# Kernel tuning notes

Measured on AMD Instinct MI355X. Metric: run time of the kernel, lower is better.

The kernel has to match this reference:

```python
import jax, jax.numpy as jnp
import numpy as np

B, T, D, H = 4, 2048, 1024, 16
HD = D // H  # 64
NEG = -np.finfo(np.float32).max


def setup_inputs() -> dict:
    key = jax.random.key(0)
    ks = jax.random.split(key, 9)
    s = 1.0 / np.sqrt(D)
    return {
        "x": jax.random.normal(ks[0], (B, T, D), jnp.float32),
        "wq": jax.random.normal(ks[1], (D, D), jnp.float32) * s,
        "bq": jax.random.normal(ks[2], (D,), jnp.float32) * 0.02,
        "wk": jax.random.normal(ks[3], (D, D), jnp.float32) * s,
        "bk": jax.random.normal(ks[4], (D,), jnp.float32) * 0.02,
        "wv": jax.random.normal(ks[5], (D, D), jnp.float32) * s,
        "bv": jax.random.normal(ks[6], (D,), jnp.float32) * 0.02,
        "wo": jax.random.normal(ks[7], (D, D), jnp.float32) * s,
        "bo": jax.random.normal(ks[8], (D,), jnp.float32) * 0.02,
    }


def reference(x, wq, bq, wk, bk, wv, bv, wo, bo):
    b, t, d = x.shape
    # separate Q, K, V projections, reshape to (B, H, T, HD)
    def proj(w, bias):
        y = x @ w + bias
        return y.reshape(b, t, H, HD).transpose(0, 2, 1, 3)
    q = proj(wq, bq)
    k = proj(wk, bk)
    v = proj(wv, bv)
    scale = 1.0 / np.sqrt(HD).astype(np.float32)
    scores = jnp.einsum("bhqd,bhkd->bhqk", q, k) * scale  # (B,H,T,T)
    # causal mask: -max_float on strictly upper triangle (matches source)
    mask = jnp.triu(jnp.full((t, t), NEG, jnp.float32), k=1)
    attn = jax.nn.softmax(scores + mask, axis=-1)
    out = jnp.einsum("bhqk,bhkd->bhqd", attn, v)
    out = out.transpose(0, 2, 1, 3).reshape(b, t, d)
    return out @ wo + bo
```

## Files before the change

### kernel.cpp

```cpp
#include <hip/hip_runtime.h>

typedef __bf16 bf16x8 __attribute__((ext_vector_type(8)));
typedef float f32x4 __attribute__((ext_vector_type(4)));

#define B_ 4
#define T_ 2048
#define D_ 1024
#define H_ 16
#define HD_ 64
#define M_ 8192
#define QSCALE 0.1803368801111204f

__device__ __forceinline__ ushort f2b(float f) {
  union { float f; unsigned u; } v; v.f = f;
  unsigned u = v.u;
  return (ushort)((u + 0x7FFFu + ((u >> 16) & 1u)) >> 16);
}

__device__ __forceinline__ unsigned pkbf(float a, float b) {
  union { float f; unsigned u; } va, vb; va.f = a; vb.f = b;
  return __builtin_amdgcn_perm(vb.u + 0x8000u, va.u + 0x8000u, 0x07060302u);
}

__device__ __forceinline__ void gll16(const void* g, void* l) {
  __builtin_amdgcn_global_load_lds(
      (const __attribute__((address_space(1))) unsigned*)g,
      (__attribute__((address_space(3))) unsigned*)l, 16, 0, 0);
}

__global__ __launch_bounds__(256) void cast_x_kernel(const float* __restrict__ x,
                                                     ushort* __restrict__ xb) {
  int idx = blockIdx.x * 256 + threadIdx.x;
  float4 v = ((const float4*)x)[idx];
  ushort4 o;
  o.x = f2b(v.x); o.y = f2b(v.y); o.z = f2b(v.z); o.w = f2b(v.w);
  ((ushort4*)xb)[idx] = o;
}

__global__ __launch_bounds__(256) void transpose_w_kernel(
    const float* __restrict__ wq, const float* __restrict__ wk,
    const float* __restrict__ wv, const float* __restrict__ wo,
    ushort* __restrict__ wt_qkv, ushort* __restrict__ wt_o) {
  __shared__ float tile[32][33];
  int z = blockIdx.z;
  const float* src = (z == 0) ? wq : (z == 1) ? wk : (z == 2) ? wv : wo;
  ushort* dst = (z < 3) ? (wt_qkv + (size_t)z * D_ * D_) : wt_o;
  int n0 = blockIdx.x * 32, k0 = blockIdx.y * 32;
  int tx = threadIdx.x & 31, ty = threadIdx.x >> 5;
  for (int i = 0; i < 4; i++) {
    int r = ty + i * 8;
    tile[r][tx] = src[(size_t)(k0 + r) * D_ + n0 + tx];
  }
  __syncthreads();
  for (int i = 0; i < 4; i++) {
    int r = ty + i * 8;
    dst[(size_t)(n0 + r) * D_ + k0 + tx] = f2b(tile[tx][r]);
  }
}

__global__ __launch_bounds__(512) void gemm_kernel(
    const ushort* __restrict__ A, const ushort* __restrict__ Bt, int mode,
    const float* __restrict__ bias_q, const float* __restrict__ bias_k,
    const float* __restrict__ bias_v,
    ushort* __restrict__ qb, ushort* __restrict__ kb, ushort* __restrict__ vtb,
    float* __restrict__ outf) {
  extern __shared__ char lds_raw[];
  ushort (*As)[256][64] = (ushort (*)[256][64])lds_raw;
  ushort (*Bs)[128][64] = (ushort (*)[128][64])(lds_raw + 98304);
  int tid = threadIdx.x;
  int wave = tid >> 6, lane = tid & 63, lrow = lane >> 4, lcol = lane & 15;
  int wr = wave >> 1, wc = wave & 1;

  int gx = gridDim.x;
  int nwg = gx * gridDim.y;
  int orig = blockIdx.x + gx * blockIdx.y;
  int work = (orig & 7) * (nwg >> 3) + (orig >> 3);
  int m0 = (work / gx) * 256, n0 = (work % gx) * 128;

  int r_s = tid >> 3, c_s = tid & 7;
  int scv = c_s ^ (r_s & 7);
  const ushort* aB = A + (size_t)(m0 + r_s) * D_ + scv * 8;
  const ushort* bB = Bt + (size_t)(n0 + r_s) * D_ + scv * 8;

  auto stageA = [&](int buf, int t, int u) {
    const ushort* s = aB + (size_t)u * 128 * D_ + t * 64;
    char* d = (char*)&As[buf][0][0] + u * 16384 + tid * 16;
    gll16(s, d);
    gll16(s + (size_t)64 * D_, d + 8192);
  };
  auto stageB = [&](int buf, int t) {
    const ushort* s = bB + t * 64;
    char* d = (char*)&Bs[buf][0][0] + tid * 16;
    gll16(s, d);
    gll16(s + (size_t)64 * D_, d + 8192);
  };

  f32x4 zero = {0.f, 0.f, 0.f, 0.f};
  f32x4 acc[4][4];
  for (int i = 0; i < 4; i++)
    for (int j = 0; j < 4; j++) acc[i][j] = zero;

  int swz = lcol & 7;

  stageA(0, 0, 0); stageA(0, 0, 1); stageB(0, 0);
  stageA(1, 1, 0); stageA(1, 1, 1); stageB(1, 1);
  asm volatile("s_waitcnt vmcnt(6)" ::: "memory");
  __builtin_amdgcn_sched_barrier(0);
  __builtin_amdgcn_s_barrier();

#pragma unroll
  for (int t = 0; t < 16; ++t) {
    int buf = t % 3;
    int nb = (t + 2) % 3;
#pragma unroll
    for (int ks = 0; ks < 2; ++ks) {
      bf16x8 af[4], bf[4];
      int ch = ((ks * 4 + lrow) ^ swz) * 8;
#pragma unroll
      for (int mt = 0; mt < 4; mt++)
        af[mt] = *(const bf16x8*)&As[buf][wr * 64 + mt * 16 + lcol][ch];
#pragma unroll
      for (int nt = 0; nt < 4; nt++)
        bf[nt] = *(const bf16x8*)&Bs[buf][wc * 64 + nt * 16 + lcol][ch];
      if (t + 2 < 16) {
        if (ks == 0) { stageA(nb, t + 2, 0); stageA(nb, t + 2, 1); }
        else         { stageB(nb, t + 2); }
      }
      __builtin_amdgcn_sched_barrier(0);
      __builtin_amdgcn_s_barrier();
      __builtin_amdgcn_sched_barrier(0);
      __builtin_amdgcn_s_setprio(1);
#pragma unroll
      for (int mt = 0; mt < 4; mt++)
#pragma unroll
        for (int nt = 0; nt < 4; nt++)
          acc[mt][nt] = __builtin_amdgcn_mfma_f32_16x16x32_bf16(
              af[mt], bf[nt], acc[mt][nt], 0, 0, 0);
      __builtin_amdgcn_s_setprio(0);
      if (ks == 1) {
        if (t <= 13) {
          asm volatile("s_waitcnt vmcnt(6)" ::: "memory");
        } else if (t == 14) {
          asm volatile("s_waitcnt vmcnt(0)" ::: "memory");
        }
      }
      __builtin_amdgcn_sched_barrier(0);
      __builtin_amdgcn_s_barrier();
    }
  }

  if (mode == 0) {
    int proj = n0 >> 10;
    const float* bias = (proj == 0) ? bias_q : (proj == 1) ? bias_k : bias_v;
    for (int mt = 0; mt < 4; mt++) {
      int gm0 = m0 + wr * 64 + mt * 16 + lrow * 4;
      int b = gm0 >> 11, tp = gm0 & 2047;
      for (int nt = 0; nt < 4; nt++) {
        int gn = n0 + wc * 64 + nt * 16 + lcol;
        int inner = gn & 1023;
        int h = inner >> 6, hd = inner & 63;
        float bv = bias[inner];
        if (proj == 0) {
          size_t base = ((size_t)(b * H_ + h) * T_ + tp) * HD_ + hd;
          for (int r = 0; r < 4; r++)
            qb[base + (size_t)r * HD_] = f2b((acc[mt][nt][r] + bv) * QSCALE);
        } else if (proj == 1) {
          size_t base = ((size_t)(b * H_ + h) * T_ + tp) * HD_ + hd;
          for (int r = 0; r < 4; r++)
            kb[base + (size_t)r * HD_] = f2b(acc[mt][nt][r] + bv);
        } else {
          ushort4 pk;
          pk.x = f2b(acc[mt][nt][0] + bv);
          pk.y = f2b(acc[mt][nt][1] + bv);
          pk.z = f2b(acc[mt][nt][2] + bv);
          pk.w = f2b(acc[mt][nt][3] + bv);
          *(ushort4*)&vtb[((size_t)(b * H_ + h) * HD_ + hd) * T_ + tp] = pk;
        }
      }
    }
  } else {
    for (int mt = 0; mt < 4; mt++) {
      int gm0 = m0 + wr * 64 + mt * 16 + lrow * 4;
      for (int nt = 0; nt < 4; nt++) {
        int gn = n0 + wc * 64 + nt * 16 + lcol;
        float bv = bias_q[gn];
        for (int r = 0; r < 4; r++)
          outf[(size_t)(gm0 + r) * D_ + gn] = acc[mt][nt][r] + bv;
      }
    }
  }
}

#define QCOMP(qblk_, q0w_, qfv, accOv, accSv)                                   \
  do {                                                                          \
    f32x4 st[2][4];                                                             \
    for (int qh = 0; qh < 2; qh++)                                              \
      for (int mt = 0; mt < 4; mt++) st[qh][mt] = zero;                         \
    __builtin_amdgcn_s_setprio(1);                                              \
    _Pragma("unroll")                                                           \
    for (int ks = 0; ks < 2; ks++)                                              \
      _Pragma("unroll")                                                         \
      for (int mt = 0; mt < 4; mt++) {                                          \
        bf16x8 kf = *(const bf16x8*)&Ks2[cur][mt * 16 + lcol]                   \
                                        [((ks * 4 + lrow) ^ rsw) * 8];          \
        st[0][mt] = __builtin_amdgcn_mfma_f32_16x16x32_bf16(kf, qfv[0][ks],     \
                                                            st[0][mt], 0, 0, 0);\
        st[1][mt] = __builtin_amdgcn_mfma_f32_16x16x32_bf16(kf, qfv[1][ks],     \
                                                            st[1][mt], 0, 0, 0);\
      }                                                                         \
    __builtin_amdgcn_s_setprio(0);                                              \
    if (j >= 2 * (qblk_)) {                                                     \
      _Pragma("unroll")                                                         \
      for (int qh = 0; qh < 2; qh++) {                                          \
        int q_g = (q0w_) + qh * 16 + lcol;                                      \
        _Pragma("unroll")                                                       \
        for (int mt = 0; mt < 4; mt++)                                          \
          for (int r = 0; r < 4; r++) {                                         \
            int kv_g = j * 64 + mt * 16 + lrow * 4 + r;                         \
            if (kv_g > q_g) st[qh][mt][r] = -1e30f;                             \
          }                                                                     \
      }                                                                         \
    }                                                                           \
    _Pragma("unroll")                                                           \
    for (int qh = 0; qh < 2; qh++)                                              \
      for (int mt = 0; mt < 4; mt++)                                            \
        for (int r = 0; r < 4; r++)                                             \
          st[qh][mt][r] = __builtin_amdgcn_exp2f(st[qh][mt][r]);                \
    _Pragma("unroll")                                                           \
    for (int qh = 0; qh < 2; qh++)                                              \
      for (int mt = 0; mt < 4; mt++) {                                          \
        uint2 pk;                                                               \
        pk.x = pkbf(st[qh][mt][0], st[qh][mt][1]);                              \
        pk.y = pkbf(st[qh][mt][2], st[qh][mt][3]);                              \
        int sl = ((2 * mt + (lrow >> 1)) ^ rsw) * 8 + (lrow & 1) * 4;           \
        *(uint2*)&Ps[wave][qh * 16 + lcol][sl] = pk;                            \
      }                                                                         \
    __builtin_amdgcn_s_setprio(1);                                              \
    _Pragma("unroll")                                                           \
    for (int ks = 0; ks < 2; ks++) {                                            \
      int ch = ((ks * 4 + lrow) ^ rsw) * 8;                                     \
      bf16x8 pf0 = *(const bf16x8*)&Ps[wave][lcol][ch];                         \
      bf16x8 pf1 = *(const bf16x8*)&Ps[wave][16 + lcol][ch];                    \
      accSv[0] = __builtin_amdgcn_mfma_f32_16x16x32_bf16(af1, pf0, accSv[0],    \
                                                         0, 0, 0);              \
      accSv[1] = __builtin_amdgcn_mfma_f32_16x16x32_bf16(af1, pf1, accSv[1],    \
                                                         0, 0, 0);              \
      _Pragma("unroll")                                                         \
      for (int mt = 0; mt < 4; mt++) {                                          \
        bf16x8 vf = *(const bf16x8*)&Vs2[cur][mt * 16 + lcol][ch];              \
        accOv[0][mt] = __builtin_amdgcn_mfma_f32_16x16x32_bf16(vf, pf0,         \
                                                    accOv[0][mt], 0, 0, 0);     \
        accOv[1][mt] = __builtin_amdgcn_mfma_f32_16x16x32_bf16(vf, pf1,         \
                                                    accOv[1][mt], 0, 0, 0);     \
      }                                                                         \
    }                                                                           \
    __builtin_amdgcn_s_setprio(0);                                              \
  } while (0)

__global__ __launch_bounds__(256) void flash_kernel(
    const ushort* __restrict__ qb, const ushort* __restrict__ kb,
    const ushort* __restrict__ vtb, ushort* __restrict__ ob) {
  __shared__ ushort Ks2[2][64][64];
  __shared__ ushort Vs2[2][64][64];
  __shared__ ushort Ps[4][32][64];
  int tid = threadIdx.x;
  int wave = tid >> 6, lane = tid & 63, lrow = lane >> 4, lcol = lane & 15;

  int bid = blockIdx.x + (blockIdx.y << 3);
  int xcd = bid & 7;
  int slot = bid >> 3;
  int phase = slot >> 5;
  int j5 = slot & 31;
  int pm = j5 & 7;
  int bh = xcd * 8 + (j5 >> 3) + phase * 4;
  int p = phase ? 7 - pm : pm;
  int qbA = 15 - p, qbB = p;
  int b = bh >> 4, h = bh & 15;
  const ushort* qp = qb + (size_t)bh * T_ * HD_;
  const ushort* kh = kb + (size_t)bh * T_ * HD_;
  const ushort* vh = vtb + (size_t)bh * HD_ * T_;

  int njA = 2 * qbA + 2, njB = 2 * qbB + 2;

  int r0 = tid >> 3, dc = tid & 7;
  int wsl = (dc ^ (r0 & 7)) * 8;
  int rsw = lcol & 7;

  uint4 kr0, kr1, vr0, vr1;
  auto gload = [&](int jt) {
    kr0 = *(const uint4*)&kh[(size_t)(jt * 64 + r0) * HD_ + dc * 8];
    kr1 = *(const uint4*)&kh[(size_t)(jt * 64 + r0 + 32) * HD_ + dc * 8];
    vr0 = *(const uint4*)&vh[(size_t)r0 * T_ + jt * 64 + dc * 8];
    vr1 = *(const uint4*)&vh[(size_t)(r0 + 32) * T_ + jt * 64 + dc * 8];
  };
  auto swrite = [&](int buf) {
    *(uint4*)&Ks2[buf][r0][wsl] = kr0;
    *(uint4*)&Ks2[buf][r0 + 32][wsl] = kr1;
    *(uint4*)&Vs2[buf][r0][wsl] = vr0;
    *(uint4*)&Vs2[buf][r0 + 32][wsl] = vr1;
  };

  bf16x8 af1;
  {
    __bf16 ov = (__bf16)((lcol == 0) ? 1.0f : 0.0f);
    for (int i2 = 0; i2 < 8; i2++) af1[i2] = ov;
  }

  f32x4 zero = {0.f, 0.f, 0.f, 0.f};

  gload(0);
  swrite(0);
  gload(1);
  __syncthreads();

  int q0wA = qbA * 128 + wave * 32, q0wB = qbB * 128 + wave * 32;
  bf16x8 qfA[2][2], qfB[2][2];
#pragma unroll
  for (int qh = 0; qh < 2; qh++)
#pragma unroll
    for (int ks = 0; ks < 2; ks++) {
      qfA[qh][ks] = *(const bf16x8*)&qp[(size_t)(q0wA + qh * 16 + lcol) * HD_ +
                                        ks * 32 + lrow * 8];
      qfB[qh][ks] = *(const bf16x8*)&qp[(size_t)(q0wB + qh * 16 + lcol) * HD_ +
                                        ks * 32 + lrow * 8];
    }

  f32x4 accOA[2][4], accOB[2][4];
  f32x4 accSA[2], accSB[2];
#pragma unroll
  for (int qh = 0; qh < 2; qh++) {
    accSA[qh] = zero; accSB[qh] = zero;
    for (int mt = 0; mt < 4; mt++) { accOA[qh][mt] = zero; accOB[qh][mt] = zero; }
  }

  for (int j = 0; j < njA; j++) {
    int cur = j & 1;
    if (j * 64 <= q0wA + 31) QCOMP(qbA, q0wA, qfA, accOA, accSA);
    if (j * 64 <= q0wB + 31) QCOMP(qbB, q0wB, qfB, accOB, accSB);
    if (j + 1 < njA) swrite(cur ^ 1);
    if (j + 2 < njA) gload(j + 2);
    __syncthreads();
  }
  (void)njB;

#pragma unroll
  for (int qh = 0; qh < 2; qh++) {
    float lsum = __shfl(accSA[qh][0], lcol);
    float linv = 1.f / lsum;
    int t = q0wA + qh * 16 + lcol;
    size_t base2 = ((size_t)b * T_ + t) * D_ + h * HD_;
#pragma unroll
    for (int mt = 0; mt < 4; mt++) {
      uint2 pk;
      pk.x = pkbf(accOA[qh][mt][0] * linv, accOA[qh][mt][1] * linv);
      pk.y = pkbf(accOA[qh][mt][2] * linv, accOA[qh][mt][3] * linv);
      *(uint2*)&ob[base2 + mt * 16 + lrow * 4] = pk;
    }
  }
#pragma unroll
  for (int qh = 0; qh < 2; qh++) {
    float lsum = __shfl(accSB[qh][0], lcol);
    float linv = 1.f / lsum;
    int t = q0wB + qh * 16 + lcol;
    size_t base2 = ((size_t)b * T_ + t) * D_ + h * HD_;
#pragma unroll
    for (int mt = 0; mt < 4; mt++) {
      uint2 pk;
      pk.x = pkbf(accOB[qh][mt][0] * linv, accOB[qh][mt][1] * linv);
      pk.y = pkbf(accOB[qh][mt][2] * linv, accOB[qh][mt][3] * linv);
      *(uint2*)&ob[base2 + mt * 16 + lrow * 4] = pk;
    }
  }
}

extern "C" void kernel_launch(void* const* d_in, const int* in_sizes, int n_in,
                              void* d_out, int out_size, void* d_ws, size_t ws_size,
                              hipStream_t stream) {
  (void)in_sizes; (void)n_in; (void)out_size; (void)ws_size;
  const float* x  = (const float*)d_in[0];
  const float* wq = (const float*)d_in[1];
  const float* bq = (const float*)d_in[2];
  const float* wk = (const float*)d_in[3];
  const float* bk = (const float*)d_in[4];
  const float* wv = (const float*)d_in[5];
  const float* bv = (const float*)d_in[6];
  const float* wo = (const float*)d_in[7];
  const float* bo = (const float*)d_in[8];
  float* out = (float*)d_out;

  char* ws = (char*)d_ws;
  ushort* xb     = (ushort*)(ws);
  ushort* wt_qkv = (ushort*)(ws + 16777216);
  ushort* wt_o   = (ushort*)(ws + 23068672);
  ushort* qb     = (ushort*)(ws + 25165824);
  ushort* kb     = (ushort*)(ws + 41943040);
  ushort* vtb    = (ushort*)(ws + 58720256);
  ushort* ob     = (ushort*)(ws + 75497472);

  hipFuncSetAttribute((const void*)gemm_kernel,
                      hipFuncAttributeMaxDynamicSharedMemorySize, 147456);

  cast_x_kernel<<<8192, 256, 0, stream>>>(x, xb);
  transpose_w_kernel<<<dim3(32, 32, 4), 256, 0, stream>>>(wq, wk, wv, wo, wt_qkv, wt_o);
  gemm_kernel<<<dim3(24, 32), 512, 147456, stream>>>(xb, wt_qkv, 0, bq, bk, bv, qb, kb, vtb, nullptr);
  flash_kernel<<<dim3(8, 64), 256, 0, stream>>>(qb, kb, vtb, ob);
  gemm_kernel<<<dim3(8, 32), 512, 147456, stream>>>(ob, wt_o, 1, bo, nullptr, nullptr,
                                                    nullptr, nullptr, nullptr, out);
}
```

Measured before the change: 256.8 us.

## Add dedicated 128x128 double-buffered GEMM kernel for output projection

```diff
diff --git a/kernel.cpp b/kernel.cpp
--- a/kernel.cpp
+++ b/kernel.cpp
@@ -58,12 +58,11 @@
   }
 }
 
-__global__ __launch_bounds__(512) void gemm_kernel(
-    const ushort* __restrict__ A, const ushort* __restrict__ Bt, int mode,
+__global__ __launch_bounds__(512) void gemm_pipe_kernel(
+    const ushort* __restrict__ A, const ushort* __restrict__ Bt,
     const float* __restrict__ bias_q, const float* __restrict__ bias_k,
     const float* __restrict__ bias_v,
-    ushort* __restrict__ qb, ushort* __restrict__ kb, ushort* __restrict__ vtb,
-    float* __restrict__ outf) {
+    ushort* __restrict__ qb, ushort* __restrict__ kb, ushort* __restrict__ vtb) {
   extern __shared__ char lds_raw[];
   ushort (*As)[256][64] = (ushort (*)[256][64])lds_raw;
   ushort (*Bs)[128][64] = (ushort (*)[128][64])(lds_raw + 98304);
@@ -149,7 +148,7 @@
     }
   }
 
-  if (mode == 0) {
+  {
     int proj = n0 >> 10;
     const float* bias = (proj == 0) ? bias_q : (proj == 1) ? bias_k : bias_v;
     for (int mt = 0; mt < 4; mt++) {
@@ -178,15 +177,73 @@
         }
       }
     }
-  } else {
-    for (int mt = 0; mt < 4; mt++) {
-      int gm0 = m0 + wr * 64 + mt * 16 + lrow * 4;
-      for (int nt = 0; nt < 4; nt++) {
-        int gn = n0 + wc * 64 + nt * 16 + lcol;
-        float bv = bias_q[gn];
-        for (int r = 0; r < 4; r++)
-          outf[(size_t)(gm0 + r) * D_ + gn] = acc[mt][nt][r] + bv;
-      }
+  }
+}
+
+__global__ __launch_bounds__(256) void gemm_o_kernel(
+    const ushort* __restrict__ A, const ushort* __restrict__ Bt,
+    const float* __restrict__ bias, float* __restrict__ outf) {
+  __shared__ ushort As[2][128][64];
+  __shared__ ushort Bs[2][128][64];
+  int tid = threadIdx.x;
+  int wave = tid >> 6, lane = tid & 63, lrow = lane >> 4, lcol = lane & 15;
+
+  int gx = gridDim.x;
+  int nwg = gx * gridDim.y;
+  int orig = blockIdx.x + gx * blockIdx.y;
+  int work = (orig & 7) * (nwg >> 3) + (orig >> 3);
+  int m0 = (work / gx) * 128, n0 = (work % gx) * 128;
+  int wm = (wave & 1) * 64, wn = (wave >> 1) * 64;
+
+  int rb = tid >> 3;
+  int dc = tid & 7;
+  int scv = dc ^ (rb & 7);
+  const ushort* aBase = A + (size_t)(m0 + rb) * D_ + scv * 8;
+  const ushort* bBase = Bt + (size_t)(n0 + rb) * D_ + scv * 8;
+
+  f32x4 zero = {0.f, 0.f, 0.f, 0.f};
+  f32x4 acc[4][4];
+  for (int i = 0; i < 4; i++)
+    for (int j = 0; j < 4; j++) acc[i][j] = zero;
+
+  int swz = lcol & 7;
+
+  auto stage = [&](int buf, int k) {
+#pragma unroll
+    for (int g = 0; g < 4; g++) {
+      gll16(aBase + (size_t)(32 * g) * D_ + k, &As[buf][0][0] + tid * 8 + g * 2048);
+      gll16(bBase + (size_t)(32 * g) * D_ + k, &Bs[buf][0][0] + tid * 8 + g * 2048);
+    }
+  };
+
+  stage(0, 0);
+
+  for (int k0 = 0; k0 < D_; k0 += 64) {
+    int cur = (k0 >> 6) & 1, nxt = cur ^ 1;
+    __syncthreads();
+    if (k0 + 64 < D_) stage(nxt, k0 + 64);
+
+    for (int ks = 0; ks < 2; ks++) {
+      bf16x8 af[4], bf[4];
+      int ch = ((ks * 4 + lrow) ^ swz) * 8;
+      for (int mt = 0; mt < 4; mt++)
+        af[mt] = *(const bf16x8*)&As[cur][wm + mt * 16 + lcol][ch];
+      for (int nt = 0; nt < 4; nt++)
+        bf[nt] = *(const bf16x8*)&Bs[cur][wn + nt * 16 + lcol][ch];
+      for (int mt = 0; mt < 4; mt++)
+        for (int nt = 0; nt < 4; nt++)
+          acc[mt][nt] = __builtin_amdgcn_mfma_f32_16x16x32_bf16(
+              af[mt], bf[nt], acc[mt][nt], 0, 0, 0);
+    }
+  }
+
+  for (int mt = 0; mt < 4; mt++) {
+    int gm0 = m0 + wm + mt * 16 + lrow * 4;
+    for (int nt = 0; nt < 4; nt++) {
+      int gn = n0 + wn + nt * 16 + lcol;
+      float bv = bias[gn];
+      for (int r = 0; r < 4; r++)
+        outf[(size_t)(gm0 + r) * D_ + gn] = acc[mt][nt][r] + bv;
     }
   }
 }
@@ -397,13 +454,13 @@
   ushort* vtb    = (ushort*)(ws + 58720256);
   ushort* ob     = (ushort*)(ws + 75497472);
 
-  hipFuncSetAttribute((const void*)gemm_kernel,
+  hipFuncSetAttribute((const void*)gemm_pipe_kernel,
                       hipFuncAttributeMaxDynamicSharedMemorySize, 147456);
 
   cast_x_kernel<<<8192, 256, 0, stream>>>(x, xb);
   transpose_w_kernel<<<dim3(32, 32, 4), 256, 0, stream>>>(wq, wk, wv, wo, wt_qkv, wt_o);
-  gemm_kernel<<<dim3(24, 32), 512, 147456, stream>>>(xb, wt_qkv, 0, bq, bk, bv, qb, kb, vtb, nullptr);
+  gemm_pipe_kernel<<<dim3(24, 32), 512, 147456, stream>>>(xb, wt_qkv, bq, bk, bv,
+                                                          qb, kb, vtb);
   flash_kernel<<<dim3(8, 64), 256, 0, stream>>>(qb, kb, vtb, ob);
-  gemm_kernel<<<dim3(8, 32), 512, 147456, stream>>>(ob, wt_o, 1, bo, nullptr, nullptr,
-                                                    nullptr, nullptr, nullptr, out);
-}
+  gemm_o_kernel<<<dim3(8, 64), 256, 0, stream>>>(ob, wt_o, bo, out);
+}
```

New measurement: 237.7 us. 7.4% less time.
